# Optimization experiments

Hardware: AMD Instinct MI355X
Metric: run time of the kernel (lower is better)

Reference implementation:

```python
import jax, jax.numpy as jnp
import numpy as np

C, B, D, Fq, T, H = 4, 2, 128, 256, 256, 4


def setup_inputs() -> dict:
    key = jax.random.key(0)
    ks = jax.random.split(key, 8)
    s = 0.05
    return {
        "h_all": jax.random.normal(ks[0], (C, B, D, Fq, T), jnp.float32),
        "ln_q_g": jnp.ones((D,), jnp.float32),
        "ln_q_b": jnp.zeros((D,), jnp.float32),
        "ln_kv_g": jnp.ones((D,), jnp.float32),
        "ln_kv_b": jnp.zeros((D,), jnp.float32),
        "Wq": jax.random.normal(ks[1], (D, D), jnp.float32) * s,
        "bq": jnp.zeros((D,), jnp.float32),
        "Wk": jax.random.normal(ks[2], (D, D), jnp.float32) * s,
        "bk": jnp.zeros((D,), jnp.float32),
        "Wv": jax.random.normal(ks[3], (D, D), jnp.float32) * s,
        "bv": jnp.zeros((D,), jnp.float32),
        "in_w": jax.random.normal(ks[4], (3 * D, D), jnp.float32) * s,
        "in_b": jnp.zeros((3 * D,), jnp.float32),
        "out_w": jax.random.normal(ks[5], (D, D), jnp.float32) * s,
        "out_b": jnp.zeros((D,), jnp.float32),
    }


def _ln(x, g, b):
    # LayerNorm over last dim, eps=1e-5 (torch default, biased variance)
    m = jnp.mean(x, axis=-1, keepdims=True)
    v = jnp.var(x, axis=-1, keepdims=True)
    return (x - m) * jax.lax.rsqrt(v + 1e-5) * g + b


def reference(h_all, ln_q_g, ln_q_b, ln_kv_g, ln_kv_b, Wq, bq, Wk, bk, Wv, bv, in_w, in_b, out_w, out_b):
    c, b_, d, f, t = h_all.shape
    h = H
    hd = d // h
    n = b_ * f * t  # flattened batch B*F*T
    # (B,d,F,T) -> (N, d) reference sequence (seq len 1 squeezed)
    h_ref_seq = jnp.transpose(h_all[0], (0, 2, 3, 1)).reshape(n, d)
    # (C,B,d,F,T) -> (N, C, d)
    h_all_seq = jnp.transpose(h_all, (1, 3, 4, 0, 2)).reshape(n, c, d)
    # module's own projections
    Q = _ln(h_ref_seq, ln_q_g, ln_q_b) @ Wq.T + bq  # (N, d)
    kv_n = _ln(h_all_seq, ln_kv_g, ln_kv_b)         # (N, C, d)
    K = kv_n @ Wk.T + bk                            # (N, C, d)
    V = kv_n @ Wv.T + bv                            # (N, C, d)
    # nn.MultiheadAttention internal in_proj (packed q/k/v) + out_proj
    q = (Q @ in_w[:d].T + in_b[:d]).reshape(n, h, hd)                    # (N,H,hd)
    k = (K @ in_w[d:2 * d].T + in_b[d:2 * d]).reshape(n, c, h, hd)       # (N,C,H,hd)
    v = (V @ in_w[2 * d:].T + in_b[2 * d:]).reshape(n, c, h, hd)         # (N,C,H,hd)
    scores = jnp.einsum('nhd,nchd->nhc', q, k) / jnp.sqrt(jnp.float32(hd))
    attn = jax.nn.softmax(scores, axis=-1)
    ctx = jnp.einsum('nhc,nchd->nhd', attn, v).reshape(n, d)
    out = ctx @ out_w.T + out_b + h_ref_seq  # residual
    return jnp.transpose(out.reshape(b_, f, t, d), (0, 3, 1, 2))  # (B,d,F,T)
```

## Files before the change

### kernel.cpp

```cpp
#include <hip/hip_runtime.h>
#include <hip/hip_bf16.h>

typedef unsigned short u16;
typedef unsigned int   u32;

#define D_ 128
#define B_ 2
#define F_ 256
#define T_ 256
#define FT (F_*T_)
#define XS 136

typedef __bf16 bf16x8 __attribute__((ext_vector_type(8)));
typedef float  floatx16 __attribute__((ext_vector_type(16)));

__device__ __forceinline__ u16 f2bf(float f) {
    union { __hip_bfloat16 h; u16 u; } cv; cv.h = __float2bfloat16(f); return cv.u;
}
__device__ __forceinline__ u32 pk2(float lo, float hi2) {
    union { __hip_bfloat162 h; u32 u; } cv;
    cv.h = __float22bfloat162_rn(make_float2(lo, hi2)); return cv.u;
}
__device__ __forceinline__ float bf2f(u16 u) { return __uint_as_float(((u32)u) << 16); }

__global__ __launch_bounds__(128) void precompute_eff(
    const float* __restrict__ lnqg, const float* __restrict__ lnqb,
    const float* __restrict__ lnkg, const float* __restrict__ lnkb,
    const float* __restrict__ Wq, const float* __restrict__ bq,
    const float* __restrict__ Wk, const float* __restrict__ bk,
    const float* __restrict__ Wv, const float* __restrict__ bv,
    const float* __restrict__ in_w, const float* __restrict__ in_b,
    const float* __restrict__ ow,
    u16* __restrict__ Agb, u16* __restrict__ Ob,
    float* __restrict__ sA, float* __restrict__ cb)
{
    const int j = blockIdx.x;
    const int sel = blockIdx.y;
    const int i = threadIdx.x;
    if (sel == 3) { Ob[j*D_ + i] = f2bf(ow[j*D_ + i]); return; }

    const float* W  = (sel==0) ? Wq : (sel==1) ? Wk : Wv;
    const float* bW = (sel==0) ? bq : (sel==1) ? bk : bv;
    const float* g  = (sel==0) ? lnqg : lnkg;
    const float* bl = (sel==0) ? lnqb : lnkb;

    __shared__ float row[D_];
    __shared__ float red[D_];
    row[i] = in_w[(sel*D_ + j)*D_ + i];
    __syncthreads();
    float acc = 0.f;
    #pragma unroll 8
    for (int m = 0; m < D_; ++m) acc = fmaf(row[m], W[m*D_ + i], acc);
    float ag = acc * g[i];
    Agb[sel*D_*D_ + j*D_ + i] = f2bf(ag);

    red[i] = ag;
    __syncthreads();
    for (int s = 64; s > 0; s >>= 1) { if (i < s) red[i] += red[i+s]; __syncthreads(); }
    if (i == 0) sA[sel*D_ + j] = red[0];
    __syncthreads();
    red[i] = acc * bl[i] + row[i] * bW[i];
    __syncthreads();
    for (int s = 64; s > 0; s >>= 1) { if (i < s) red[i] += red[i+s]; __syncthreads(); }
    if (i == 0) cb[sel*D_ + j] = red[0] + in_b[sel*D_ + j];
}

__global__ __launch_bounds__(256, 3) void cca_mfma(
    const float* __restrict__ h,
    const u16*  __restrict__ Agb,
    const u16*  __restrict__ Ob,
    const float* __restrict__ sA,
    const float* __restrict__ cbp,
    const float* __restrict__ out_b,
    float* __restrict__ outp)
{
    __shared__ __align__(16) u16 xb[4][32*XS];
    __shared__ __align__(16) u16 ctxb[32*XS];
    __shared__ float  swt[4][4][32];
    __shared__ float2 stf[4][32];

    const int tid = threadIdx.x;
    const int blk = blockIdx.x;
    const int t0 = (blk & 7) * 32;
    const int f  = (blk >> 3) & 255;
    const int b  = blk >> 11;

    {
        const int dd = tid >> 3;
        const int t4 = (tid & 7) * 4;
        #pragma unroll
        for (int it = 0; it < 2; ++it) {
            const int d = 2*dd + 64*it;
            #pragma unroll
            for (int c = 0; c < 4; ++c) {
                const float* p = h + ((size_t)((c*B_ + b)*D_ + d))*FT + (size_t)f*T_ + t0 + t4;
                float4 v0 = *(const float4*)p;
                float4 v1 = *(const float4*)(p + FT);
                u32* dst = (u32*)xb[c] + dd + 32*it;
                dst[(size_t)(t4+0)*(XS/2)] = pk2(v0.x, v1.x);
                dst[(size_t)(t4+1)*(XS/2)] = pk2(v0.y, v1.y);
                dst[(size_t)(t4+2)*(XS/2)] = pk2(v0.z, v1.z);
                dst[(size_t)(t4+3)*(XS/2)] = pk2(v0.w, v1.w);
            }
        }
    }
    __syncthreads();

    if (tid < 128) {
        const int c = tid >> 5, t = tid & 31;
        const u32* row = (const u32*)(xb[c] + t*XS);
        float s = 0.f, sq = 0.f;
        #pragma unroll
        for (int i = 0; i < 16; ++i) {
            uint4 w = *(const uint4*)(row + i*4);
            const u32 us[4] = {w.x, w.y, w.z, w.w};
            #pragma unroll
            for (int k = 0; k < 4; ++k) {
                float lo = __uint_as_float(us[k] << 16);
                float hi = __uint_as_float(us[k] & 0xffff0000u);
                s += lo + hi;
                sq = fmaf(lo, lo, fmaf(hi, hi, sq));
            }
        }
        float m = s * (1.f/128.f);
        float var = fmaf(-m, m, sq * (1.f/128.f));
        stf[c][t] = make_float2(m, rsqrtf(var + 1e-5f));
    }
    __syncthreads();

    const int wv  = tid >> 6;
    const int l   = tid & 63;
    const int lo5 = l & 31, hi = l >> 5;
    const int jq  = wv*32 + lo5;
    const int xoff = lo5*XS + hi*8;

    const u16* Bq = Agb +            (size_t)jq*D_ + hi*8;
    const u16* Bk = Agb + 16384 +    (size_t)jq*D_ + hi*8;
    const u16* Bv = Agb + 32768 +    (size_t)jq*D_ + hi*8;
    const u16* Bo = Ob  +            (size_t)jq*D_ + hi*8;
    const float sAq = sA[jq],      cbq = cbp[jq];
    const float sAk = sA[128+jq],  cbk = cbp[128+jq];
    const float sAv = sA[256+jq],  cbv = cbp[256+jq];

    auto gemm32 = [&](const u16* X, const u16* Bp) {
        floatx16 acc;
        #pragma unroll
        for (int i = 0; i < 16; ++i) acc[i] = 0.f;
        #pragma unroll
        for (int ks = 0; ks < 8; ++ks) {
            bf16x8 a  = *(const bf16x8*)(X + xoff + ks*16);
            bf16x8 bb = *(const bf16x8*)(Bp + ks*16);
            acc = __builtin_amdgcn_mfma_f32_32x32x16_bf16(a, bb, acc, 0, 0, 0);
        }
        return acc;
    };
    auto fold = [&](floatx16& acc, int c, float sAx, float cbx) {
        #pragma unroll
        for (int i = 0; i < 16; ++i) {
            const int t = (i&3) + 8*(i>>2) + 4*hi;
            float2 mr = stf[c][t];
            acc[i] = fmaf(mr.y, fmaf(-mr.x, sAx, acc[i]), cbx);
        }
    };

    floatx16 qv = gemm32(xb[0], Bq);
    fold(qv, 0, sAq, cbq);

    #pragma unroll
    for (int c = 0; c < 4; ++c) {
        floatx16 kv = gemm32(xb[c], Bk);
        fold(kv, c, sAk, cbk);
        floatx16 p;
        #pragma unroll
        for (int i = 0; i < 16; ++i) p[i] = qv[i] * kv[i];
        #pragma unroll
        for (int msk = 1; msk <= 16; msk <<= 1) {
            #pragma unroll
            for (int i = 0; i < 16; ++i) p[i] += __shfl_xor(p[i], msk);
        }
        if (lo5 == 0) {
            #pragma unroll
            for (int i = 0; i < 16; ++i)
                swt[wv][c][(i&3) + 8*(i>>2) + 4*hi] = p[i] * 0.17677669529663687f;
        }
    }

    #pragma unroll
    for (int i = 0; i < 16; ++i) {
        const int t = (i&3) + 8*(i>>2) + 4*hi;
        float s0 = swt[wv][0][t], s1 = swt[wv][1][t];
        float s2 = swt[wv][2][t], s3 = swt[wv][3][t];
        float mm = fmaxf(fmaxf(s0, s1), fmaxf(s2, s3));
        float e0 = __expf(s0-mm), e1 = __expf(s1-mm);
        float e2 = __expf(s2-mm), e3 = __expf(s3-mm);
        float inv = 1.f / (e0+e1+e2+e3);
        if (lo5 == 0) {
            swt[wv][0][t] = e0*inv; swt[wv][1][t] = e1*inv;
            swt[wv][2][t] = e2*inv; swt[wv][3][t] = e3*inv;
        }
    }

    floatx16 ctx;
    #pragma unroll
    for (int i = 0; i < 16; ++i) ctx[i] = 0.f;
    #pragma unroll
    for (int c = 0; c < 4; ++c) {
        floatx16 vv = gemm32(xb[c], Bv);
        fold(vv, c, sAv, cbv);
        #pragma unroll
        for (int i = 0; i < 16; ++i) {
            const int t = (i&3) + 8*(i>>2) + 4*hi;
            ctx[i] = fmaf(swt[wv][c][t], vv[i], ctx[i]);
        }
    }

    #pragma unroll
    for (int i = 0; i < 16; ++i) {
        const int t = (i&3) + 8*(i>>2) + 4*hi;
        ctxb[t*XS + jq] = f2bf(ctx[i]);
    }
    __syncthreads();

    floatx16 o = gemm32(ctxb, Bo);
    const float obv = out_b[jq];
    float* obase = outp + ((size_t)(b*D_ + jq))*FT + (size_t)f*T_ + t0;
    #pragma unroll
    for (int g = 0; g < 4; ++g) {
        const int tb = 8*g + 4*hi;
        float4 st;
        st.x = o[g*4+0] + obv + bf2f(xb[0][(tb+0)*XS + jq]);
        st.y = o[g*4+1] + obv + bf2f(xb[0][(tb+1)*XS + jq]);
        st.z = o[g*4+2] + obv + bf2f(xb[0][(tb+2)*XS + jq]);
        st.w = o[g*4+3] + obv + bf2f(xb[0][(tb+3)*XS + jq]);
        *(float4*)(obase + tb) = st;
    }
}

extern "C" void kernel_launch(void* const* d_in, const int* in_sizes, int n_in,
                              void* d_out, int out_size, void* d_ws, size_t ws_size,
                              hipStream_t stream) {
    const float* h    = (const float*)d_in[0];
    const float* lnqg = (const float*)d_in[1];
    const float* lnqb = (const float*)d_in[2];
    const float* lnkg = (const float*)d_in[3];
    const float* lnkb = (const float*)d_in[4];
    const float* Wq   = (const float*)d_in[5];
    const float* bq   = (const float*)d_in[6];
    const float* Wk   = (const float*)d_in[7];
    const float* bk   = (const float*)d_in[8];
    const float* Wv   = (const float*)d_in[9];
    const float* bv   = (const float*)d_in[10];
    const float* in_w = (const float*)d_in[11];
    const float* in_b = (const float*)d_in[12];
    const float* ow   = (const float*)d_in[13];
    const float* ob   = (const float*)d_in[14];

    char* ws = (char*)d_ws;
    u16*   Agb = (u16*)ws;
    u16*   Obf = (u16*)(ws + 98304);
    float* sAe = (float*)(ws + 98304 + 32768);
    float* cbe = (float*)(ws + 98304 + 32768 + 1536);

    precompute_eff<<<dim3(128, 4), 128, 0, stream>>>(
        lnqg, lnqb, lnkg, lnkb, Wq, bq, Wk, bk, Wv, bv,
        in_w, in_b, ow, Agb, Obf, sAe, cbe);
    cca_mfma<<<dim3(B_*F_*(T_/32)), 256, 0, stream>>>(
        h, Agb, Obf, sAe, cbe, ob, (float*)d_out);
}
```

Baseline: 479.1 us.

## Compute per-head attention scores with MFMA and pre-scale inputs by LayerNorm rstd

Each bf16 row in shared memory is pre-scaled in place by its LayerNorm rstd, so the fold after each GEMM shrinks to one add. The 32-lane shuffle reduction for q·k scores is replaced by staging q and k tiles into a small shared buffer and running an MFMA whose diagonal gives the per-head scores. The K and V GEMMs are batched across channels so the weight fragments are loaded once. The ctx buffer reuses xb[1], and the residual is rebuilt by multiplying by the stored inverse rstd. This adds bf16 rounding of the rstd-scaled values and of q and k before scoring, and relies on manual lgkmcnt waits in place of block barriers.

```diff
diff --git a/kernel.cpp b/kernel.cpp
--- a/kernel.cpp
+++ b/kernel.cpp
@@ -10,9 +10,12 @@
 #define T_ 256
 #define FT (F_*T_)
 #define XS 136
+#define QS 40
 
 typedef __bf16 bf16x8 __attribute__((ext_vector_type(8)));
 typedef float  floatx16 __attribute__((ext_vector_type(16)));
+
+#define LGKM0 asm volatile("s_waitcnt lgkmcnt(0)" ::: "memory")
 
 __device__ __forceinline__ u16 f2bf(float f) {
     union { __hip_bfloat16 h; u16 u; } cv; cv.h = __float2bfloat16(f); return cv.u;
@@ -75,9 +78,10 @@
     float* __restrict__ outp)
 {
     __shared__ __align__(16) u16 xb[4][32*XS];
-    __shared__ __align__(16) u16 ctxb[32*XS];
-    __shared__ float  swt[4][4][32];
-    __shared__ float2 stf[4][32];
+    __shared__ __align__(16) u16 qk[4][32*QS];
+    __shared__ float swt[4][4][32];
+    __shared__ float rmneg[4][32];
+    __shared__ float invr[32];
 
     const int tid = threadIdx.x;
     const int blk = blockIdx.x;
@@ -106,25 +110,42 @@
     }
     __syncthreads();
 
-    if (tid < 128) {
-        const int c = tid >> 5, t = tid & 31;
-        const u32* row = (const u32*)(xb[c] + t*XS);
+    {
+        const int rowi = tid >> 1, half = tid & 1;
+        const int c = rowi >> 5, t = rowi & 31;
+        u32* rowp = (u32*)(xb[c] + t*XS) + half*32;
+        u32 rw[32];
+        #pragma unroll
+        for (int i = 0; i < 8; ++i) {
+            uint4 q = ((const uint4*)rowp)[i];
+            rw[4*i] = q.x; rw[4*i+1] = q.y; rw[4*i+2] = q.z; rw[4*i+3] = q.w;
+        }
         float s = 0.f, sq = 0.f;
         #pragma unroll
-        for (int i = 0; i < 16; ++i) {
-            uint4 w = *(const uint4*)(row + i*4);
-            const u32 us[4] = {w.x, w.y, w.z, w.w};
-            #pragma unroll
-            for (int k = 0; k < 4; ++k) {
-                float lo = __uint_as_float(us[k] << 16);
-                float hi = __uint_as_float(us[k] & 0xffff0000u);
-                s += lo + hi;
-                sq = fmaf(lo, lo, fmaf(hi, hi, sq));
-            }
-        }
+        for (int k = 0; k < 32; ++k) {
+            float lo = __uint_as_float(rw[k] << 16);
+            float hi2 = __uint_as_float(rw[k] & 0xffff0000u);
+            s += lo + hi2;
+            sq = fmaf(lo, lo, fmaf(hi2, hi2, sq));
+        }
+        s += __shfl_xor(s, 1);
+        sq += __shfl_xor(sq, 1);
         float m = s * (1.f/128.f);
         float var = fmaf(-m, m, sq * (1.f/128.f));
-        stf[c][t] = make_float2(m, rsqrtf(var + 1e-5f));
+        float r = rsqrtf(var + 1e-5f);
+        #pragma unroll
+        for (int i = 0; i < 8; ++i) {
+            uint4 q;
+            q.x = pk2(__uint_as_float(rw[4*i]   << 16)*r, __uint_as_float(rw[4*i]   & 0xffff0000u)*r);
+            q.y = pk2(__uint_as_float(rw[4*i+1] << 16)*r, __uint_as_float(rw[4*i+1] & 0xffff0000u)*r);
+            q.z = pk2(__uint_as_float(rw[4*i+2] << 16)*r, __uint_as_float(rw[4*i+2] & 0xffff0000u)*r);
+            q.w = pk2(__uint_as_float(rw[4*i+3] << 16)*r, __uint_as_float(rw[4*i+3] & 0xffff0000u)*r);
+            ((uint4*)rowp)[i] = q;
+        }
+        if (half == 0) {
+            rmneg[c][t] = -r*m;
+            if (c == 0) invr[t] = 1.0f / r;
+        }
     }
     __syncthreads();
 
@@ -132,106 +153,169 @@
     const int l   = tid & 63;
     const int lo5 = l & 31, hi = l >> 5;
     const int jq  = wv*32 + lo5;
-    const int xoff = lo5*XS + hi*8;
-
-    const u16* Bq = Agb +            (size_t)jq*D_ + hi*8;
-    const u16* Bk = Agb + 16384 +    (size_t)jq*D_ + hi*8;
-    const u16* Bv = Agb + 32768 +    (size_t)jq*D_ + hi*8;
-    const u16* Bo = Ob  +            (size_t)jq*D_ + hi*8;
+    u16* qkw = qk[wv];
+    const int xoff  = lo5*XS + hi*8;
+    const int qkoff = lo5*QS + hi*8;
+
+    const u16* Bq = Agb +         (size_t)jq*D_ + hi*8;
+    const u16* Bk = Agb + 16384 + (size_t)jq*D_ + hi*8;
+    const u16* Bv = Agb + 32768 + (size_t)jq*D_ + hi*8;
+    const u16* Bo = Ob  +         (size_t)jq*D_ + hi*8;
     const float sAq = sA[jq],      cbq = cbp[jq];
     const float sAk = sA[128+jq],  cbk = cbp[128+jq];
     const float sAv = sA[256+jq],  cbv = cbp[256+jq];
 
-    auto gemm32 = [&](const u16* X, const u16* Bp) {
-        floatx16 acc;
-        #pragma unroll
-        for (int i = 0; i < 16; ++i) acc[i] = 0.f;
-        #pragma unroll
-        for (int ks = 0; ks < 8; ++ks) {
-            bf16x8 a  = *(const bf16x8*)(X + xoff + ks*16);
-            bf16x8 bb = *(const bf16x8*)(Bp + ks*16);
-            acc = __builtin_amdgcn_mfma_f32_32x32x16_bf16(a, bb, acc, 0, 0, 0);
-        }
-        return acc;
+    auto foldv = [&](floatx16& a, int c, float sAx, float cbx) {
+        #pragma unroll
+        for (int g = 0; g < 4; ++g) {
+            float4 rm4 = *(const float4*)&rmneg[c][8*g + 4*hi];
+            a[4*g+0] += fmaf(rm4.x, sAx, cbx);
+            a[4*g+1] += fmaf(rm4.y, sAx, cbx);
+            a[4*g+2] += fmaf(rm4.z, sAx, cbx);
+            a[4*g+3] += fmaf(rm4.w, sAx, cbx);
+        }
     };
-    auto fold = [&](floatx16& acc, int c, float sAx, float cbx) {
+    auto stage = [&](const floatx16& a) {
         #pragma unroll
         for (int i = 0; i < 16; ++i) {
             const int t = (i&3) + 8*(i>>2) + 4*hi;
-            float2 mr = stf[c][t];
-            acc[i] = fmaf(mr.y, fmaf(-mr.x, sAx, acc[i]), cbx);
+            qkw[t*QS + lo5] = f2bf(a[i]);
         }
     };
-
-    floatx16 qv = gemm32(xb[0], Bq);
-    fold(qv, 0, sAq, cbq);
-
+    auto diag = [&](const floatx16& s2) -> float {
+        const bool b0 = lo5 & 1, b1 = lo5 & 2, b2 = lo5 & 8, b3 = lo5 & 16;
+        float t01 = b0 ? s2[1] : s2[0],  t23 = b0 ? s2[3] : s2[2];
+        float t45 = b0 ? s2[5] : s2[4],  t67 = b0 ? s2[7] : s2[6];
+        float t89 = b0 ? s2[9] : s2[8],  tab = b0 ? s2[11] : s2[10];
+        float tcd = b0 ? s2[13] : s2[12], tef = b0 ? s2[15] : s2[14];
+        float u0 = b1 ? t23 : t01, u1 = b1 ? t67 : t45;
+        float u2 = b1 ? tab : t89, u3 = b1 ? tef : tcd;
+        float v0 = b2 ? u1 : u0,  v1 = b2 ? u3 : u2;
+        return b3 ? v1 : v0;
+    };
+
+    floatx16 qa;
+    #pragma unroll
+    for (int i = 0; i < 16; ++i) qa[i] = 0.f;
+    #pragma unroll
+    for (int ks = 0; ks < 8; ++ks) {
+        bf16x8 a  = *(const bf16x8*)(xb[0] + xoff + ks*16);
+        bf16x8 bb = *(const bf16x8*)(Bq + ks*16);
+        qa = __builtin_amdgcn_mfma_f32_32x32x16_bf16(a, bb, qa, 0, 0, 0);
+    }
+    foldv(qa, 0, sAq, cbq);
+    stage(qa);
+    LGKM0;
+    bf16x8 qf0 = *(const bf16x8*)(qkw + qkoff);
+    bf16x8 qf1 = *(const bf16x8*)(qkw + qkoff + 16);
+    LGKM0;
+
+    floatx16 ka0, ka1, ka2, ka3;
+    #pragma unroll
+    for (int i = 0; i < 16; ++i) { ka0[i]=0.f; ka1[i]=0.f; ka2[i]=0.f; ka3[i]=0.f; }
+    #pragma unroll
+    for (int ks = 0; ks < 8; ++ks) {
+        bf16x8 bb = *(const bf16x8*)(Bk + ks*16);
+        bf16x8 a0 = *(const bf16x8*)(xb[0] + xoff + ks*16);
+        bf16x8 a1 = *(const bf16x8*)(xb[1] + xoff + ks*16);
+        bf16x8 a2 = *(const bf16x8*)(xb[2] + xoff + ks*16);
+        bf16x8 a3 = *(const bf16x8*)(xb[3] + xoff + ks*16);
+        ka0 = __builtin_amdgcn_mfma_f32_32x32x16_bf16(a0, bb, ka0, 0, 0, 0);
+        ka1 = __builtin_amdgcn_mfma_f32_32x32x16_bf16(a1, bb, ka1, 0, 0, 0);
+        ka2 = __builtin_amdgcn_mfma_f32_32x32x16_bf16(a2, bb, ka2, 0, 0, 0);
+        ka3 = __builtin_amdgcn_mfma_f32_32x32x16_bf16(a3, bb, ka3, 0, 0, 0);
+    }
+    float sreg[4];
     #pragma unroll
     for (int c = 0; c < 4; ++c) {
-        floatx16 kv = gemm32(xb[c], Bk);
-        fold(kv, c, sAk, cbk);
-        floatx16 p;
-        #pragma unroll
-        for (int i = 0; i < 16; ++i) p[i] = qv[i] * kv[i];
-        #pragma unroll
-        for (int msk = 1; msk <= 16; msk <<= 1) {
+        floatx16& ka = (c==0) ? ka0 : (c==1) ? ka1 : (c==2) ? ka2 : ka3;
+        foldv(ka, c, sAk, cbk);
+        stage(ka);
+        LGKM0;
+        bf16x8 kf0 = *(const bf16x8*)(qkw + qkoff);
+        bf16x8 kf1 = *(const bf16x8*)(qkw + qkoff + 16);
+        LGKM0;
+        floatx16 sc;
+        #pragma unroll
+        for (int i = 0; i < 16; ++i) sc[i] = 0.f;
+        sc = __builtin_amdgcn_mfma_f32_32x32x16_bf16(qf0, kf0, sc, 0, 0, 0);
+        sc = __builtin_amdgcn_mfma_f32_32x32x16_bf16(qf1, kf1, sc, 0, 0, 0);
+        sreg[c] = diag(sc) * 0.17677669529663687f;
+    }
+
+    {
+        const bool active = (hi == ((lo5 >> 2) & 1));
+        if (active) {
+            float mm = fmaxf(fmaxf(sreg[0], sreg[1]), fmaxf(sreg[2], sreg[3]));
+            float e0 = __expf(sreg[0]-mm), e1 = __expf(sreg[1]-mm);
+            float e2 = __expf(sreg[2]-mm), e3 = __expf(sreg[3]-mm);
+            float inv = 1.f / (e0+e1+e2+e3);
+            swt[wv][0][lo5] = e0*inv; swt[wv][1][lo5] = e1*inv;
+            swt[wv][2][lo5] = e2*inv; swt[wv][3][lo5] = e3*inv;
+        }
+    }
+    LGKM0;
+
+    floatx16 ctx;
+    #pragma unroll
+    for (int i = 0; i < 16; ++i) ctx[i] = 0.f;
+    #pragma unroll
+    for (int cp = 0; cp < 4; cp += 2) {
+        floatx16 va0, va1;
+        #pragma unroll
+        for (int i = 0; i < 16; ++i) { va0[i]=0.f; va1[i]=0.f; }
+        #pragma unroll
+        for (int ks = 0; ks < 8; ++ks) {
+            bf16x8 bb = *(const bf16x8*)(Bv + ks*16);
+            bf16x8 a0 = *(const bf16x8*)(xb[cp]   + xoff + ks*16);
+            bf16x8 a1 = *(const bf16x8*)(xb[cp+1] + xoff + ks*16);
+            va0 = __builtin_amdgcn_mfma_f32_32x32x16_bf16(a0, bb, va0, 0, 0, 0);
+            va1 = __builtin_amdgcn_mfma_f32_32x32x16_bf16(a1, bb, va1, 0, 0, 0);
+        }
+        #pragma unroll
+        for (int d = 0; d < 2; ++d) {
+            const int c = cp + d;
+            floatx16& va = d ? va1 : va0;
+            foldv(va, c, sAv, cbv);
             #pragma unroll
-            for (int i = 0; i < 16; ++i) p[i] += __shfl_xor(p[i], msk);
-        }
-        if (lo5 == 0) {
-            #pragma unroll
-            for (int i = 0; i < 16; ++i)
-                swt[wv][c][(i&3) + 8*(i>>2) + 4*hi] = p[i] * 0.17677669529663687f;
-        }
-    }
-
+            for (int g = 0; g < 4; ++g) {
+                float4 w4 = *(const float4*)&swt[wv][c][8*g + 4*hi];
+                ctx[4*g+0] = fmaf(w4.x, va[4*g+0], ctx[4*g+0]);
+                ctx[4*g+1] = fmaf(w4.y, va[4*g+1], ctx[4*g+1]);
+                ctx[4*g+2] = fmaf(w4.z, va[4*g+2], ctx[4*g+2]);
+                ctx[4*g+3] = fmaf(w4.w, va[4*g+3], ctx[4*g+3]);
+            }
+        }
+    }
+
+    __syncthreads();
     #pragma unroll
     for (int i = 0; i < 16; ++i) {
         const int t = (i&3) + 8*(i>>2) + 4*hi;
-        float s0 = swt[wv][0][t], s1 = swt[wv][1][t];
-        float s2 = swt[wv][2][t], s3 = swt[wv][3][t];
-        float mm = fmaxf(fmaxf(s0, s1), fmaxf(s2, s3));
-        float e0 = __expf(s0-mm), e1 = __expf(s1-mm);
-        float e2 = __expf(s2-mm), e3 = __expf(s3-mm);
-        float inv = 1.f / (e0+e1+e2+e3);
-        if (lo5 == 0) {
-            swt[wv][0][t] = e0*inv; swt[wv][1][t] = e1*inv;
-            swt[wv][2][t] = e2*inv; swt[wv][3][t] = e3*inv;
-        }
-    }
-
-    floatx16 ctx;
-    #pragma unroll
-    for (int i = 0; i < 16; ++i) ctx[i] = 0.f;
-    #pragma unroll
-    for (int c = 0; c < 4; ++c) {
-        floatx16 vv = gemm32(xb[c], Bv);
-        fold(vv, c, sAv, cbv);
-        #pragma unroll
-        for (int i = 0; i < 16; ++i) {
-            const int t = (i&3) + 8*(i>>2) + 4*hi;
-            ctx[i] = fmaf(swt[wv][c][t], vv[i], ctx[i]);
-        }
-    }
-
-    #pragma unroll
-    for (int i = 0; i < 16; ++i) {
-        const int t = (i&3) + 8*(i>>2) + 4*hi;
-        ctxb[t*XS + jq] = f2bf(ctx[i]);
-    }
-    __syncthreads();
-
-    floatx16 o = gemm32(ctxb, Bo);
+        xb[1][t*XS + jq] = f2bf(ctx[i]);
+    }
+    __syncthreads();
+
+    floatx16 oa;
+    #pragma unroll
+    for (int i = 0; i < 16; ++i) oa[i] = 0.f;
+    #pragma unroll
+    for (int ks = 0; ks < 8; ++ks) {
+        bf16x8 a  = *(const bf16x8*)(xb[1] + xoff + ks*16);
+        bf16x8 bb = *(const bf16x8*)(Bo + ks*16);
+        oa = __builtin_amdgcn_mfma_f32_32x32x16_bf16(a, bb, oa, 0, 0, 0);
+    }
     const float obv = out_b[jq];
     float* obase = outp + ((size_t)(b*D_ + jq))*FT + (size_t)f*T_ + t0;
     #pragma unroll
     for (int g = 0; g < 4; ++g) {
         const int tb = 8*g + 4*hi;
+        float4 iv4 = *(const float4*)&invr[tb];
         float4 st;
-        st.x = o[g*4+0] + obv + bf2f(xb[0][(tb+0)*XS + jq]);
-        st.y = o[g*4+1] + obv + bf2f(xb[0][(tb+1)*XS + jq]);
-        st.z = o[g*4+2] + obv + bf2f(xb[0][(tb+2)*XS + jq]);
-        st.w = o[g*4+3] + obv + bf2f(xb[0][(tb+3)*XS + jq]);
+        st.x = oa[g*4+0] + obv + bf2f(xb[0][(tb+0)*XS + jq]) * iv4.x;
+        st.y = oa[g*4+1] + obv + bf2f(xb[0][(tb+1)*XS + jq]) * iv4.y;
+        st.z = oa[g*4+2] + obv + bf2f(xb[0][(tb+2)*XS + jq]) * iv4.z;
+        st.w = oa[g*4+3] + obv + bf2f(xb[0][(tb+3)*XS + jq]) * iv4.w;
         *(float4*)(obase + tb) = st;
     }
 }
```

Result: faster. 467.7 us (-2.4%).
